# Kernel tuning notes

Measured on AMD Instinct MI355X. Metric: run time of the kernel, lower is better.

## Reference

```python
import jax, jax.numpy as jnp
import numpy as np
from jax import lax

CONF_TH = 0.9
NMS_TH = 0.5


def setup_inputs() -> dict:
    key = jax.random.key(0)
    predictions = jax.random.normal(key, (32, 22743, 85), dtype=jnp.float32)
    return {"predictions": predictions, "max_det": 512}


def _xywh2xyxy(b):
    cx, cy, w, h = b[..., 0], b[..., 1], b[..., 2], b[..., 3]
    return jnp.stack([cx - w / 2, cy - h / 2, cx + w / 2, cy + h / 2], axis=-1)


def _pairwise_iou(boxes):
    # boxes: [K, 4] xyxy
    area = jnp.clip(boxes[:, 2] - boxes[:, 0], 0) * jnp.clip(boxes[:, 3] - boxes[:, 1], 0)
    lt = jnp.maximum(boxes[:, None, :2], boxes[None, :, :2])
    rb = jnp.minimum(boxes[:, None, 2:], boxes[None, :, 2:])
    wh = jnp.clip(rb - lt, 0)
    inter = wh[..., 0] * wh[..., 1]
    union = area[:, None] + area[None, :] - inter
    return inter / jnp.maximum(union, 1e-9)


def _nms_keep(boxes, cls_id, valid, K):
    # boxes sorted by descending score; greedy class-aware suppression
    iou = _pairwise_iou(boxes)                       # [K, K]
    same_cls = cls_id[:, None] == cls_id[None, :]
    suppress = (iou > NMS_TH) & same_cls
    later = jnp.arange(K)

    def body(i, keep):
        sup_i = keep[i] & suppress[i] & (later > i)
        return keep & ~sup_i

    return lax.fori_loop(0, K, body, valid)


def _predict(predictions, K):
    B = predictions.shape[0]
    boxes = _xywh2xyxy(predictions[..., :4])          # [B, N, 4]
    scores = jax.nn.sigmoid(predictions[..., 4:])     # [B, N, 1+C]
    obj = scores[..., 0]                              # [B, N]
    cls = scores[..., 1:]                             # [B, N, C]

    # confidence filter via masking + fixed-size top-k (static shapes)
    masked = jnp.where(obj >= CONF_TH, obj, -1.0)
    top_obj, idx = lax.top_k(masked, K)               # [B, K], sorted desc
    valid = top_obj >= CONF_TH

    boxes_k = jnp.take_along_axis(boxes, idx[..., None], axis=1)   # [B, K, 4]
    obj_k = jnp.take_along_axis(obj, idx, axis=1)                  # [B, K]
    cls_k = jnp.take_along_axis(cls, idx[..., None], axis=1)       # [B, K, C]
    cls_conf = cls_k.max(-1)                                       # [B, K]
    cls_id = cls_k.argmax(-1)                                      # [B, K]

    keep = jax.vmap(lambda b, c, v: _nms_keep(b, c, v, K))(boxes_k, cls_id, valid)

    dets = jnp.concatenate(
        [boxes_k, obj_k[..., None], cls_conf[..., None], cls_id[..., None].astype(jnp.float32)],
        axis=-1,
    )                                                              # [B, K, 7]
    dets = dets * keep[..., None].astype(dets.dtype)
    return dets, keep


def reference(predictions, max_det):
    return _predict(predictions, max_det)
```

## Files before the change

kernel.cpp:

```cpp
#include <hip/hip_runtime.h>

#define CONF_TH 0.9f
#define NMS_TH  0.5f
#define KDET    512
#define CAP     1024
#define NCLS    80
#define CH      85
#define NBATCH  32

typedef unsigned long long ull;

__global__ void yolo_zero(int* __restrict__ cnt) {
    if (threadIdx.x < NBATCH) cnt[threadIdx.x] = 0;
}

__global__ void yolo_scan(const float* __restrict__ pred, int A, int cap,
                          ull* __restrict__ cand, int* __restrict__ cnt)
{
    const int b = blockIdx.y;
    const int a = blockIdx.x * blockDim.x + threadIdx.x;
    if (a >= A) return;
    float logit = pred[((size_t)b * A + a) * CH + 4];
    float obj = 1.0f / (1.0f + expf(-logit));
    if (obj >= CONF_TH) {
        int pos = atomicAdd(&cnt[b], 1);
        if (pos < cap) {
            cand[(size_t)b * CAP + pos] =
                ((ull)__float_as_uint(obj) << 32) | (ull)(~(unsigned)a);
        }
    }
}

__global__ __launch_bounds__(1024) void yolo_finalize(
    const float* __restrict__ pred, int A, int cap,
    const ull* __restrict__ cand, const int* __restrict__ cnt_g,
    float* __restrict__ out_dets,
    float* __restrict__ out_keep)
{
    const int b = blockIdx.x;
    const int tid = threadIdx.x;
    const float* __restrict__ p = pred + (size_t)b * A * CH;

    __shared__ ull keys[CAP];
    __shared__ ull skeys[KDET];
    __shared__ float bx1[KDET], by1[KDET], bx2[KDET], by2[KDET];
    __shared__ float s_obj[KDET], s_conf[KDET];
    __shared__ int   s_cls[KDET];
    __shared__ unsigned sup[KDET][16];
    __shared__ unsigned keepw[KDET / 32];

    int cnt = cnt_g[b];
    if (cnt > cap) cnt = cap;
    const int nval = cnt < KDET ? cnt : KDET;

    if (tid < cnt) keys[tid] = cand[(size_t)b * CAP + tid];
    __syncthreads();

    if (tid < cnt) {
        ull key = keys[tid];
        int rank = 0;
        for (int j = 0; j < cnt; ++j) rank += (keys[j] > key) ? 1 : 0;
        if (rank < KDET) skeys[rank] = key;
    }
    #pragma unroll
    for (int i = 0; i < (KDET * 16) / 1024; ++i)
        ((unsigned*)sup)[tid + i * 1024] = 0u;
    __syncthreads();

    if (tid < KDET) {
        const int k = tid;
        if (k < nval) {
            ull key = skeys[k];
            int a = (int)(~(unsigned)(key & 0xFFFFFFFFull));
            const float* __restrict__ row = p + (size_t)a * CH;
            float cx = row[0], cy = row[1], w = row[2], h = row[3];
            bx1[k] = cx - w * 0.5f;
            by1[k] = cy - h * 0.5f;
            bx2[k] = cx + w * 0.5f;
            by2[k] = cy + h * 0.5f;
            float best = row[5];
            int bid = 0;
            #pragma unroll 4
            for (int c = 1; c < NCLS; ++c) {
                float v = row[5 + c];
                if (v > best) { best = v; bid = c; }
            }
            s_conf[k] = 1.0f / (1.0f + expf(-best));
            s_cls[k]  = bid;
            s_obj[k]  = __uint_as_float((unsigned)(key >> 32));
        } else {
            bx1[k] = 0.f; by1[k] = 0.f; bx2[k] = 0.f; by2[k] = 0.f;
            s_obj[k] = 0.f; s_conf[k] = 0.f; s_cls[k] = 0;
        }
    }
    __syncthreads();

    if (tid < nval) {
        const int i = tid;
        float x1 = bx1[i], y1 = by1[i], x2 = bx2[i], y2 = by2[i];
        int   ci = s_cls[i];
        float ai = fmaxf(x2 - x1, 0.f) * fmaxf(y2 - y1, 0.f);
        for (int j = i + 1; j < nval; ++j) {
            if (s_cls[j] != ci) continue;
            float jx1 = bx1[j], jy1 = by1[j], jx2 = bx2[j], jy2 = by2[j];
            float aj = fmaxf(jx2 - jx1, 0.f) * fmaxf(jy2 - jy1, 0.f);
            float xx1 = fmaxf(x1, jx1), yy1 = fmaxf(y1, jy1);
            float xx2 = fminf(x2, jx2), yy2 = fminf(y2, jy2);
            float ww = fmaxf(xx2 - xx1, 0.f), hh = fmaxf(yy2 - yy1, 0.f);
            float inter = ww * hh;
            float uni = ai + aj - inter;
            float iou = inter / fmaxf(uni, 1e-9f);
            if (iou > NMS_TH) sup[i][j >> 5] |= (1u << (j & 31));
        }
    }
    __syncthreads();

    if (tid < 64) {
        const int l = tid;
        unsigned keep_w;
        if ((l + 1) * 32 <= nval)      keep_w = 0xFFFFFFFFu;
        else if (l * 32 >= nval)       keep_w = 0u;
        else                           keep_w = (1u << (nval - l * 32)) - 1u;
        for (int i = 0; i < nval; ++i) {
            int w = i >> 5;
            unsigned kb = (unsigned)__shfl((int)keep_w, w);
            unsigned sw = (l < 16) ? sup[i][l] : 0u;
            unsigned mask = ((kb >> (i & 31)) & 1u) ? ~sw : 0xFFFFFFFFu;
            keep_w &= mask;
        }
        if (l < KDET / 32) keepw[l] = keep_w;
    }
    __syncthreads();

    if (tid < KDET) {
        const int k = tid;
        float kp = ((keepw[k >> 5] >> (k & 31)) & 1u) ? 1.0f : 0.0f;
        float* d = out_dets + ((size_t)b * KDET + k) * 7;
        d[0] = bx1[k] * kp;
        d[1] = by1[k] * kp;
        d[2] = bx2[k] * kp;
        d[3] = by2[k] * kp;
        d[4] = s_obj[k]  * kp;
        d[5] = s_conf[k] * kp;
        d[6] = (float)s_cls[k] * kp;
        out_keep[(size_t)b * KDET + k] = kp;
    }
}

extern "C" void kernel_launch(void* const* d_in, const int* in_sizes, int n_in,
                              void* d_out, int out_size, void* d_ws, size_t ws_size,
                              hipStream_t stream) {
    const float* pred = (const float*)d_in[0];
    const int A = in_sizes[0] / (NBATCH * CH);

    int* cnt  = (int*)d_ws;
    ull* cand = (ull*)((char*)d_ws + 256);
    size_t need = 256 + (size_t)NBATCH * CAP * sizeof(ull);
    int cap = CAP;
    if (ws_size < need) {
        size_t per = (ws_size > 256 ? ws_size - 256 : 0) / (NBATCH * sizeof(ull));
        cap = per < (size_t)CAP ? (int)per : CAP;
    }

    yolo_zero<<<1, 64, 0, stream>>>(cnt);

    dim3 sg((A + 255) / 256, NBATCH);
    yolo_scan<<<sg, 256, 0, stream>>>(pred, A, cap, cand, cnt);

    float* dets = (float*)d_out;
    float* keep = dets + (size_t)NBATCH * KDET * 7;
    yolo_finalize<<<NBATCH, 1024, 0, stream>>>(pred, A, cap, cand, cnt, dets, keep);
}
```

Baseline: 174.8 us.

## Split candidate decoding into separate kernel and unroll scan over four anchors per thread

Candidate box decoding and the class argmax over 80 logits move out of the sort/NMS kernel into a new decode kernel. It writes packed 8-float records to workspace, which the finalize kernel scatters by rank. The decode no longer waits behind the O(n^2) rank sort and can overlap its gather latency across all candidates rather than only the top 512. The scan kernel now handles four anchors per thread, so each block issues more loads in flight. The cost is an extra launch and workspace traffic, and the workspace-size fallback check is dropped, so it assumes ws_size is large enough.

```diff
diff --git a/kernel.cpp b/kernel.cpp
--- a/kernel.cpp
+++ b/kernel.cpp
@@ -14,35 +14,82 @@
     if (threadIdx.x < NBATCH) cnt[threadIdx.x] = 0;
 }
 
-__global__ void yolo_scan(const float* __restrict__ pred, int A, int cap,
-                          ull* __restrict__ cand, int* __restrict__ cnt)
+__global__ __launch_bounds__(256) void yolo_scan(
+    const float* __restrict__ pred, int A, int cap,
+    ull* __restrict__ cand, int* __restrict__ cnt)
 {
     const int b = blockIdx.y;
-    const int a = blockIdx.x * blockDim.x + threadIdx.x;
-    if (a >= A) return;
-    float logit = pred[((size_t)b * A + a) * CH + 4];
-    float obj = 1.0f / (1.0f + expf(-logit));
-    if (obj >= CONF_TH) {
-        int pos = atomicAdd(&cnt[b], 1);
-        if (pos < cap) {
-            cand[(size_t)b * CAP + pos] =
-                ((ull)__float_as_uint(obj) << 32) | (ull)(~(unsigned)a);
-        }
-    }
-}
-
-__global__ __launch_bounds__(1024) void yolo_finalize(
+    const int a0 = blockIdx.x * 1024 + threadIdx.x;
+    const float* __restrict__ pb = pred + (size_t)b * A * CH + 4;
+
+    float lg[4];
+    #pragma unroll
+    for (int u = 0; u < 4; ++u) {
+        int a = a0 + u * 256;
+        lg[u] = (a < A) ? pb[(size_t)a * CH] : -100.0f;
+    }
+    #pragma unroll
+    for (int u = 0; u < 4; ++u) {
+        float obj = 1.0f / (1.0f + expf(-lg[u]));
+        if (obj >= CONF_TH) {
+            int a = a0 + u * 256;
+            int pos = atomicAdd(&cnt[b], 1);
+            if (pos < cap) {
+                cand[(size_t)b * CAP + pos] =
+                    ((ull)__float_as_uint(obj) << 32) | (ull)(~(unsigned)a);
+            }
+        }
+    }
+}
+
+__global__ __launch_bounds__(1024) void yolo_decode(
     const float* __restrict__ pred, int A, int cap,
     const ull* __restrict__ cand, const int* __restrict__ cnt_g,
+    float* __restrict__ rec)
+{
+    const int b = blockIdx.x;
+    const int t = threadIdx.x;
+    int cnt = cnt_g[b];
+    if (cnt > cap) cnt = cap;
+    if (t >= cnt) return;
+
+    ull key = cand[(size_t)b * CAP + t];
+    int a = (int)(~(unsigned)(key & 0xFFFFFFFFull));
+    const float* __restrict__ row = pred + ((size_t)b * A + a) * CH;
+
+    float cx = row[0], cy = row[1], w = row[2], h = row[3];
+    float best = row[5];
+    int bid = 0;
+    #pragma unroll 4
+    for (int c = 1; c < NCLS; ++c) {
+        float v = row[5 + c];
+        if (v > best) { best = v; bid = c; }
+    }
+    float4 r0, r1;
+    r0.x = cx - w * 0.5f;
+    r0.y = cy - h * 0.5f;
+    r0.z = cx + w * 0.5f;
+    r0.w = cy + h * 0.5f;
+    r1.x = __uint_as_float((unsigned)(key >> 32));
+    r1.y = 1.0f / (1.0f + expf(-best));
+    r1.z = (float)bid;
+    r1.w = 0.0f;
+    float4* out = (float4*)(rec + ((size_t)b * CAP + t) * 8);
+    out[0] = r0;
+    out[1] = r1;
+}
+
+__global__ __launch_bounds__(1024) void yolo_finalize(
+    int cap,
+    const ull* __restrict__ cand, const int* __restrict__ cnt_g,
+    const float* __restrict__ rec,
     float* __restrict__ out_dets,
     float* __restrict__ out_keep)
 {
     const int b = blockIdx.x;
     const int tid = threadIdx.x;
-    const float* __restrict__ p = pred + (size_t)b * A * CH;
 
     __shared__ ull keys[CAP];
-    __shared__ ull skeys[KDET];
     __shared__ float bx1[KDET], by1[KDET], bx2[KDET], by2[KDET];
     __shared__ float s_obj[KDET], s_conf[KDET];
     __shared__ int   s_cls[KDET];
@@ -54,43 +101,26 @@
     const int nval = cnt < KDET ? cnt : KDET;
 
     if (tid < cnt) keys[tid] = cand[(size_t)b * CAP + tid];
+    if (tid < KDET) {
+        bx1[tid] = 0.f; by1[tid] = 0.f; bx2[tid] = 0.f; by2[tid] = 0.f;
+        s_obj[tid] = 0.f; s_conf[tid] = 0.f; s_cls[tid] = 0;
+    }
+    #pragma unroll
+    for (int i = 0; i < (KDET * 16) / 1024; ++i)
+        ((unsigned*)sup)[tid + i * 1024] = 0u;
     __syncthreads();
 
     if (tid < cnt) {
         ull key = keys[tid];
         int rank = 0;
         for (int j = 0; j < cnt; ++j) rank += (keys[j] > key) ? 1 : 0;
-        if (rank < KDET) skeys[rank] = key;
-    }
-    #pragma unroll
-    for (int i = 0; i < (KDET * 16) / 1024; ++i)
-        ((unsigned*)sup)[tid + i * 1024] = 0u;
-    __syncthreads();
-
-    if (tid < KDET) {
-        const int k = tid;
-        if (k < nval) {
-            ull key = skeys[k];
-            int a = (int)(~(unsigned)(key & 0xFFFFFFFFull));
-            const float* __restrict__ row = p + (size_t)a * CH;
-            float cx = row[0], cy = row[1], w = row[2], h = row[3];
-            bx1[k] = cx - w * 0.5f;
-            by1[k] = cy - h * 0.5f;
-            bx2[k] = cx + w * 0.5f;
-            by2[k] = cy + h * 0.5f;
-            float best = row[5];
-            int bid = 0;
-            #pragma unroll 4
-            for (int c = 1; c < NCLS; ++c) {
-                float v = row[5 + c];
-                if (v > best) { best = v; bid = c; }
-            }
-            s_conf[k] = 1.0f / (1.0f + expf(-best));
-            s_cls[k]  = bid;
-            s_obj[k]  = __uint_as_float((unsigned)(key >> 32));
-        } else {
-            bx1[k] = 0.f; by1[k] = 0.f; bx2[k] = 0.f; by2[k] = 0.f;
-            s_obj[k] = 0.f; s_conf[k] = 0.f; s_cls[k] = 0;
+        if (rank < KDET) {
+            const float4* r = (const float4*)(rec + ((size_t)b * CAP + tid) * 8);
+            float4 r0 = r[0], r1 = r[1];
+            bx1[rank] = r0.x; by1[rank] = r0.y;
+            bx2[rank] = r0.z; by2[rank] = r0.w;
+            s_obj[rank] = r1.x; s_conf[rank] = r1.y;
+            s_cls[rank] = (int)r1.z;
         }
     }
     __syncthreads();
@@ -153,21 +183,19 @@
     const float* pred = (const float*)d_in[0];
     const int A = in_sizes[0] / (NBATCH * CH);
 
-    int* cnt  = (int*)d_ws;
-    ull* cand = (ull*)((char*)d_ws + 256);
-    size_t need = 256 + (size_t)NBATCH * CAP * sizeof(ull);
+    int*   cnt  = (int*)d_ws;
+    ull*   cand = (ull*)((char*)d_ws + 256);
+    float* rec  = (float*)((char*)d_ws + 256 + (size_t)NBATCH * CAP * sizeof(ull));
     int cap = CAP;
-    if (ws_size < need) {
-        size_t per = (ws_size > 256 ? ws_size - 256 : 0) / (NBATCH * sizeof(ull));
-        cap = per < (size_t)CAP ? (int)per : CAP;
-    }
 
     yolo_zero<<<1, 64, 0, stream>>>(cnt);
 
-    dim3 sg((A + 255) / 256, NBATCH);
+    dim3 sg((A + 1023) / 1024, NBATCH);
     yolo_scan<<<sg, 256, 0, stream>>>(pred, A, cap, cand, cnt);
+
+    yolo_decode<<<NBATCH, 1024, 0, stream>>>(pred, A, cap, cand, cnt, rec);
 
     float* dets = (float*)d_out;
     float* keep = dets + (size_t)NBATCH * KDET * 7;
-    yolo_finalize<<<NBATCH, 1024, 0, stream>>>(pred, A, cap, cand, cnt, dets, keep);
-}
+    yolo_finalize<<<NBATCH, 1024, 0, stream>>>(cap, cand, cnt, rec, dets, keep);
+}
```

After: 152.2 us. 12.9% less time.
